# Performance work log

Measured on AMD Instinct MI355X. Metric: run time of the kernel, lower is better.

Reference implementation:

```python
import jax, jax.numpy as jnp
import numpy as np

B, S, J, D = 64, 2048, 25, 3
FEAT_DIM = 128
COMPUTED = 12  # pos(3) + vel(3) + acc(3) + angles(3)
IN_MLP = COMPUTED * J  # 300
HID = FEAT_DIM * 2     # 256
CONN = np.array([(0, 1), (1, 5), (1, 6), (5, 7), (7, 9), (6, 8), (8, 10),
                 (1, 11), (1, 12), (11, 13), (13, 15), (12, 14), (14, 16)], dtype=np.int32)


def setup_inputs() -> dict:
    key = jax.random.key(0)
    ks = jax.random.split(key, 8)
    return {
        "poses": jax.random.normal(ks[0], (B, S, J, D), dtype=jnp.float32),
        "W1": jax.random.normal(ks[1], (IN_MLP, HID), dtype=jnp.float32) * 0.05,
        "b1": jnp.zeros((HID,), jnp.float32),
        "gamma": jnp.ones((HID,), jnp.float32),
        "beta": jnp.zeros((HID,), jnp.float32),
        "running_mean": jnp.zeros((HID,), jnp.float32),
        "running_var": jnp.ones((HID,), jnp.float32),
        "W2": jax.random.normal(ks[2], (HID, FEAT_DIM), dtype=jnp.float32) * 0.05,
        "b2": jnp.zeros((FEAT_DIM,), jnp.float32),
        "joint_weights": jnp.ones((J,), jnp.float32),
    }


def reference(poses, W1, b1, gamma, beta, running_mean, running_var, W2, b2, joint_weights):
    b, s, j, d = poses.shape
    # --- root-centering + max-distance normalization ---
    p = poses - poses[:, :, 0:1, :]
    dist = jnp.linalg.norm(p, axis=-1, keepdims=True)           # [B,S,J,1]
    max_dist = jnp.max(dist, axis=2, keepdims=True)             # [B,S,1,1]
    p = p / (max_dist + 1e-8)
    # --- velocity / acceleration (zero-padded first frames) ---
    zpad = jnp.zeros_like(p[:, :1])
    vel = jnp.concatenate([zpad, p[:, 1:] - p[:, :-1]], axis=1)
    acc = jnp.concatenate([zpad, vel[:, 1:] - vel[:, :-1]], axis=1)
    # --- joint angles: vectorized gather + normalize + acos (replaces B*S*13 python loop) ---
    v1 = p[:, :, CONN[:, 1], :] - p[:, :, CONN[:, 0], :]        # [B,S,13,3]
    vnorm = jnp.maximum(jnp.linalg.norm(v1, axis=-1, keepdims=True), 1e-12)  # F.normalize eps
    ang = jnp.arccos(jnp.clip(v1 / vnorm, -1.0, 1.0))           # [B,S,13,3]
    ang = ang.reshape(b, s, -1)                                 # [B,S,39]
    pad = jnp.zeros((b, s, j * 3 - ang.shape[-1]), ang.dtype)   # pad to J*3=75
    angles = jnp.concatenate([ang, pad], axis=-1).reshape(b, s, j, 3)
    # --- combine, weight, project ---
    feat = jnp.concatenate([p, vel, acc, angles], axis=-1)      # [B,S,J,12]
    feat = feat * joint_weights.reshape(1, 1, j, 1)
    x = feat.reshape(b * s, -1)                                 # [B*S,300]
    x = x @ W1 + b1
    x = gamma * (x - running_mean) / jnp.sqrt(running_var + 1e-5) + beta  # BN eval mode
    x = jax.nn.relu(x)                                          # dropout = identity (eval)
    x = x @ W2 + b2
    return x.reshape(b, s, -1)                                  # [B,S,128]
```

## Files before the change

### kernel.cpp

```cpp
#include <hip/hip_runtime.h>
#include <hip/hip_bf16.h>
#include <stdint.h>


#define S_    2048
#define MT_   64
#define HID_  256
#define OUT_  128

typedef __attribute__((ext_vector_type(8))) short   short8;
typedef __attribute__((ext_vector_type(4))) float   floatx4;

#define C0M 0x0ECDB118675110ULL
#define C1M 0x0FDECBA9786540ULL

__device__ __forceinline__ unsigned short bf16_bits(float v) {
    union { float f; unsigned u; } x; x.f = v;
    unsigned r = x.u + 0x7fffu + ((x.u >> 16) & 1u);
    return (unsigned short)(r >> 16);
}

__device__ __forceinline__ unsigned pkbf16(float a, float b) {
#if __has_builtin(__builtin_amdgcn_cvt_pk_bf16_f32)
    auto v = __builtin_amdgcn_cvt_pk_bf16_f32(a, b);
    unsigned u; __builtin_memcpy(&u, &v, 4); return u;
#else
    return (unsigned)bf16_bits(a) | ((unsigned)bf16_bits(b) << 16);
#endif
}

__device__ __forceinline__ float facos(float x) {
    float ax = fabsf(x);
    float p = fmaf(ax, -0.0187293f, 0.0742610f);
    p = fmaf(ax, p, -0.2121144f);
    p = fmaf(ax, p, 1.5707288f);
    float r = __builtin_amdgcn_sqrtf(1.f - ax) * p;
    return x < 0.f ? 3.14159265358979f - r : r;
}

__global__ void prep_kernel(const float* __restrict__ W1, const float* __restrict__ b1,
                            const float* __restrict__ gamma, const float* __restrict__ beta,
                            const float* __restrict__ rmean, const float* __restrict__ rvar,
                            const float* __restrict__ W2,
                            unsigned short* __restrict__ w1p,
                            unsigned short* __restrict__ w2p,
                            float* __restrict__ b1p) {
    int idx = blockIdx.x * 256 + threadIdx.x;
    if (idx < 81920) {
        int k = idx >> 8, n = idx & 255;
        float a = gamma[n] * __builtin_amdgcn_rsqf(rvar[n] + 1e-5f);
        float v = (k < 300) ? W1[k * HID_ + n] * a : 0.f;
        int blk = (k >> 5) * 16 + (n >> 4);
        int off = blk * 512 + (((k >> 3) & 3) * 16 + (n & 15)) * 8 + (k & 7);
        w1p[off] = bf16_bits(v);
    } else if (idx < 114688) {
        int i2 = idx - 81920;
        int k = i2 >> 7, n = i2 & 127;
        int blk = (k >> 5) * 8 + (n >> 4);
        int off = blk * 512 + (((k >> 3) & 3) * 16 + (n & 15)) * 8 + (k & 7);
        w2p[off] = bf16_bits(W2[k * OUT_ + n]);
    } else if (idx < 114944) {
        int n = idx - 114688;
        float a = gamma[n] * __builtin_amdgcn_rsqf(rvar[n] + 1e-5f);
        b1p[n] = fmaf(a, b1[n] - rmean[n], beta[n]);
    }
}

#define LDS_FEAT 0
#define LDS_PB   41984
#define LDS_RSM  (LDS_PB + 34 * 76 * 4)
#define LDS_JW   (LDS_RSM + 34 * 4)
#define LDS_TOT  (LDS_JW + 25 * 4 + 4)

__global__ __launch_bounds__(256, 3) void pose_mlp(
    const float* __restrict__ poses,
    const unsigned short* __restrict__ w1p,
    const unsigned short* __restrict__ w2p,
    const float* __restrict__ b1p,
    const float* __restrict__ b2,
    const float* __restrict__ jw,
    float* __restrict__ out)
{
    __shared__ __align__(16) unsigned char smem[LDS_TOT];
    const int tid  = threadIdx.x;
    const int lane = tid & 63;
    const int wv   = tid >> 6;
    const int t0   = blockIdx.x * MT_;
    const int s0   = t0 & (S_ - 1);

    unsigned short* feat = (unsigned short*)(smem + LDS_FEAT);
    float*    pbuf = (float*)(smem + LDS_PB);
    unsigned* rsm  = (unsigned*)(smem + LDS_RSM);
    float*    scl  = (float*)rsm;
    float*    jwl  = (float*)(smem + LDS_JW);

    short8 bw[4];
    #pragma unroll
    for (int ni = 0; ni < 4; ni++)
        bw[ni] = *(const short8*)(w1p + (unsigned)(wv * 4 + ni) * 512 + lane * 8);

    if (tid < 25) jwl[tid] = jw[tid];
    for (int i = tid; i < MT_ * 64; i += 256) {
        int tt = i >> 6, z = i & 63;
        int k;
        if (z < 36) { int jj = z / 3; k = (13 + jj) * 12 + 9 + (z - jj * 3); }
        else        { k = 300 + z - 36; }
        feat[tt * 328 + k] = 0;
    }

    for (int h = 0; h < 2; h++) {
        int hb = t0 + 32 * h - 2;
        if (tid < 34) rsm[tid] = 0u;
        for (int i = tid; i < 34 * 75; i += 256) {
            int f = i / 75, r = i - f * 75;
            int g = hb + f; if (g < 0) g = 0;
            const float* P = poses + (size_t)g * 75;
            pbuf[f * 76 + r] = P[r] - P[r - (r / 3) * 3];
        }
        __syncthreads();
        for (int i = tid; i < 34 * 25; i += 256) {
            int f = i / 25, j = i - f * 25;
            const float* q = pbuf + f * 76 + j * 3;
            float d2 = fmaf(q[0], q[0], fmaf(q[1], q[1], q[2] * q[2]));
            atomicMax(&rsm[f], __float_as_uint(d2));
        }
        __syncthreads();
        if (tid < 34) {
            float m = __uint_as_float(rsm[tid]);
            scl[tid] = __builtin_amdgcn_rcpf(__builtin_amdgcn_sqrtf(m) + 1e-8f);
        }
        __syncthreads();
        for (int i = tid; i < 32 * 25; i += 256) {
            int tt = i / 25, j = i - tt * 25;
            int s  = s0 + 32 * h + tt;
            const float* pc = pbuf + (tt + 2) * 76 + j * 3;
            const float* pm = pc - 76;
            const float* pp = pc - 152;
            float sc = scl[tt + 2], sm = scl[tt + 1], sp = scl[tt];
            float cx = pc[0] * sc, cy = pc[1] * sc, cz = pc[2] * sc;
            float mx = pm[0] * sm, my = pm[1] * sm, mz = pm[2] * sm;
            float px = pp[0] * sp, py = pp[1] * sp, pz = pp[2] * sp;
            bool h1 = (s >= 1), h2 = (s >= 2);
            float vx = h1 ? cx - mx : 0.f, vy = h1 ? cy - my : 0.f, vz = h1 ? cz - mz : 0.f;
            float ux = h2 ? mx - px : 0.f, uy = h2 ? my - py : 0.f, uz = h2 ? mz - pz : 0.f;
            float qx = vx - ux, qy = vy - uy, qz = vz - uz;
            float w = jwl[j];
            unsigned base = (unsigned)(32 * h + tt) * 328 + j * 12;
            *(unsigned*)(feat + base)     = pkbf16(cx * w, cy * w);
            *(unsigned*)(feat + base + 2) = pkbf16(cz * w, vx * w);
            *(unsigned*)(feat + base + 4) = pkbf16(vy * w, vz * w);
            *(unsigned*)(feat + base + 6) = pkbf16(qx * w, qy * w);
            feat[base + 8] = bf16_bits(qz * w);
        }
        for (int i = tid; i < 32 * 13; i += 256) {
            int tt = i / 13, e = i - tt * 13;
            const float* pf = pbuf + (tt + 2) * 76;
            int a0 = (int)((C0M >> (4 * e)) & 15) * 3;
            int a1 = (((int)((C1M >> (4 * e)) & 15)) + 1) * 3;
            float vx = pf[a1] - pf[a0], vy = pf[a1+1] - pf[a0+1], vz = pf[a1+2] - pf[a0+2];
            float d  = fmaf(vx, vx, fmaf(vy, vy, vz * vz));
            float inv = __builtin_amdgcn_rcpf(fmaxf(__builtin_amdgcn_sqrtf(d), 1e-12f));
            float w = jwl[e];
            float A0 = facos(fminf(fmaxf(vx * inv, -1.f), 1.f)) * w;
            float A1 = facos(fminf(fmaxf(vy * inv, -1.f), 1.f)) * w;
            float A2 = facos(fminf(fmaxf(vz * inv, -1.f), 1.f)) * w;
            unsigned base = (unsigned)(32 * h + tt) * 328 + e * 12 + 9;
            feat[base] = bf16_bits(A0);
            *(unsigned*)(feat + base + 1) = pkbf16(A1, A2);
        }
        __syncthreads();
    }

    floatx4 acc[4][4];
    #pragma unroll
    for (int mi = 0; mi < 4; mi++)
        #pragma unroll
        for (int ni = 0; ni < 4; ni++) acc[mi][ni] = (floatx4){0.f, 0.f, 0.f, 0.f};

    #pragma unroll 1
    for (int kc = 0; kc < 10; kc++) {
        short8 bn[4];
        if (kc < 9) {
            #pragma unroll
            for (int ni = 0; ni < 4; ni++)
                bn[ni] = *(const short8*)(w1p + (unsigned)((kc + 1) * 16 + wv * 4 + ni) * 512 + lane * 8);
        }
        short8 af[4];
        #pragma unroll
        for (int mi = 0; mi < 4; mi++)
            af[mi] = *(const short8*)(feat + (mi * 16 + (lane & 15)) * 328 + kc * 32 + (lane >> 4) * 8);
        #pragma unroll
        for (int mi = 0; mi < 4; mi++)
            #pragma unroll
            for (int ni = 0; ni < 4; ni++)
                acc[mi][ni] = __builtin_amdgcn_mfma_f32_16x16x32_bf16(
                    af[mi], bw[ni], acc[mi][ni], 0, 0, 0);
        if (kc < 9) {
            #pragma unroll
            for (int ni = 0; ni < 4; ni++) bw[ni] = bn[ni];
        }
    }

    short8 bw2[2];
    #pragma unroll
    for (int ni = 0; ni < 2; ni++)
        bw2[ni] = *(const short8*)(w2p + (unsigned)(wv * 2 + ni) * 512 + lane * 8);

    __syncthreads();

    unsigned short* hid = feat;
    float bv[4];
    #pragma unroll
    for (int ni = 0; ni < 4; ni++) bv[ni] = b1p[wv * 64 + ni * 16 + (lane & 15)];
    #pragma unroll
    for (int mi = 0; mi < 4; mi++)
        #pragma unroll
        for (int ni = 0; ni < 4; ni++)
            #pragma unroll
            for (int r = 0; r < 4; r++) {
                float v = fmaxf(acc[mi][ni][r] + bv[ni], 0.f);
                int m   = mi * 16 + (lane >> 4) * 4 + r;
                int col = wv * 64 + ni * 16 + (lane & 15);
                hid[m * 264 + col] = bf16_bits(v);
            }
    __syncthreads();

    floatx4 acc2[4][2];
    #pragma unroll
    for (int mi = 0; mi < 4; mi++)
        #pragma unroll
        for (int ni = 0; ni < 2; ni++) acc2[mi][ni] = (floatx4){0.f, 0.f, 0.f, 0.f};

    #pragma unroll 1
    for (int kc = 0; kc < 8; kc++) {
        short8 bn2[2];
        if (kc < 7) {
            #pragma unroll
            for (int ni = 0; ni < 2; ni++)
                bn2[ni] = *(const short8*)(w2p + (unsigned)((kc + 1) * 8 + wv * 2 + ni) * 512 + lane * 8);
        }
        short8 af[4];
        #pragma unroll
        for (int mi = 0; mi < 4; mi++)
            af[mi] = *(const short8*)(hid + (mi * 16 + (lane & 15)) * 264 + kc * 32 + (lane >> 4) * 8);
        #pragma unroll
        for (int mi = 0; mi < 4; mi++)
            #pragma unroll
            for (int ni = 0; ni < 2; ni++)
                acc2[mi][ni] = __builtin_amdgcn_mfma_f32_16x16x32_bf16(
                    af[mi], bw2[ni], acc2[mi][ni], 0, 0, 0);
        if (kc < 7) {
            #pragma unroll
            for (int ni = 0; ni < 2; ni++) bw2[ni] = bn2[ni];
        }
    }

    float c2[2];
    #pragma unroll
    for (int ni = 0; ni < 2; ni++) c2[ni] = b2[wv * 32 + ni * 16 + (lane & 15)];
    #pragma unroll
    for (int mi = 0; mi < 4; mi++)
        #pragma unroll
        for (int ni = 0; ni < 2; ni++)
            #pragma unroll
            for (int r = 0; r < 4; r++) {
                int m   = mi * 16 + (lane >> 4) * 4 + r;
                int col = wv * 32 + ni * 16 + (lane & 15);
                out[(size_t)(t0 + m) * OUT_ + col] = acc2[mi][ni][r] + c2[ni];
            }
}

extern "C" void kernel_launch(void* const* d_in, const int* in_sizes, int n_in,
                              void* d_out, int out_size, void* d_ws, size_t ws_size,
                              hipStream_t stream) {
    (void)in_sizes; (void)n_in; (void)out_size; (void)ws_size;
    const float* poses = (const float*)d_in[0];
    const float* W1    = (const float*)d_in[1];
    const float* b1    = (const float*)d_in[2];
    const float* gamma = (const float*)d_in[3];
    const float* beta  = (const float*)d_in[4];
    const float* rmean = (const float*)d_in[5];
    const float* rvar  = (const float*)d_in[6];
    const float* W2    = (const float*)d_in[7];
    const float* b2    = (const float*)d_in[8];
    const float* jw    = (const float*)d_in[9];

    unsigned short* w1p = (unsigned short*)d_ws;
    unsigned short* w2p = w1p + 320 * HID_;
    float* b1p = (float*)((char*)d_ws + (320 * HID_ + HID_ * OUT_) * 2);

    prep_kernel<<<449, 256, 0, stream>>>(W1, b1, gamma, beta, rmean, rvar, W2,
                                         w1p, w2p, b1p);
    pose_mlp<<<2048, 256, 0, stream>>>(poses, w1p, w2p, b1p, b2, jw, (float*)d_out);
}
```

Measured before the change: 174.5 us.

## Use 512-thread blocks and compute pose features directly from global memory

Doubles the block to 8 waves, so each wave covers half as many output columns in both GEMMs (2 N-tiles instead of 4 for layer 1, 1 instead of 2 for layer 2). Feature construction moves from two staged 32-frame halves with an LDS pose buffer and atomicMax to one pass over all 66 frames. That pass computes a partial max per 5-joint group plus a per-frame root and scale record, then reads poses from global/L1 directly. The goal is fewer barriers and less LDS traffic, with more waves to hide latency. In exchange there are redundant global loads of poses, and each wave now re-reads the same A fragments for fewer MFMAs.

```diff
diff --git a/kernel.cpp b/kernel.cpp
--- a/kernel.cpp
+++ b/kernel.cpp
@@ -5,6 +5,7 @@
 
 #define S_    2048
 #define MT_   64
+#define TPB   512
 #define HID_  256
 #define OUT_  128
 
@@ -67,12 +68,12 @@
 }
 
 #define LDS_FEAT 0
-#define LDS_PB   41984
-#define LDS_RSM  (LDS_PB + 34 * 76 * 4)
-#define LDS_JW   (LDS_RSM + 34 * 4)
-#define LDS_TOT  (LDS_JW + 25 * 4 + 4)
-
-__global__ __launch_bounds__(256, 3) void pose_mlp(
+#define LDS_PM   41984
+#define LDS_RS   43312
+#define LDS_JW   (LDS_RS + 66 * 16)
+#define LDS_TOT  (LDS_JW + 25 * 4 + 12)
+
+__global__ __launch_bounds__(TPB, 6) void pose_mlp(
     const float* __restrict__ poses,
     const unsigned short* __restrict__ w1p,
     const unsigned short* __restrict__ w2p,
@@ -89,18 +90,17 @@
     const int s0   = t0 & (S_ - 1);
 
     unsigned short* feat = (unsigned short*)(smem + LDS_FEAT);
-    float*    pbuf = (float*)(smem + LDS_PB);
-    unsigned* rsm  = (unsigned*)(smem + LDS_RSM);
-    float*    scl  = (float*)rsm;
-    float*    jwl  = (float*)(smem + LDS_JW);
-
-    short8 bw[4];
-    #pragma unroll
-    for (int ni = 0; ni < 4; ni++)
-        bw[ni] = *(const short8*)(w1p + (unsigned)(wv * 4 + ni) * 512 + lane * 8);
+    float*  pm  = (float*)(smem + LDS_PM);
+    float4* rs  = (float4*)(smem + LDS_RS);
+    float*  jwl = (float*)(smem + LDS_JW);
+
+    short8 bw[2];
+    #pragma unroll
+    for (int ni = 0; ni < 2; ni++)
+        bw[ni] = *(const short8*)(w1p + (unsigned)(wv * 2 + ni) * 512 + lane * 8);
 
     if (tid < 25) jwl[tid] = jw[tid];
-    for (int i = tid; i < MT_ * 64; i += 256) {
+    for (int i = tid; i < MT_ * 64; i += TPB) {
         int tt = i >> 6, z = i & 63;
         int k;
         if (z < 36) { int jj = z / 3; k = (13 + jj) * 12 + 9 + (z - jj * 3); }
@@ -108,82 +108,91 @@
         feat[tt * 328 + k] = 0;
     }
 
-    for (int h = 0; h < 2; h++) {
-        int hb = t0 + 32 * h - 2;
-        if (tid < 34) rsm[tid] = 0u;
-        for (int i = tid; i < 34 * 75; i += 256) {
-            int f = i / 75, r = i - f * 75;
-            int g = hb + f; if (g < 0) g = 0;
-            const float* P = poses + (size_t)g * 75;
-            pbuf[f * 76 + r] = P[r] - P[r - (r / 3) * 3];
-        }
-        __syncthreads();
-        for (int i = tid; i < 34 * 25; i += 256) {
-            int f = i / 25, j = i - f * 25;
-            const float* q = pbuf + f * 76 + j * 3;
-            float d2 = fmaf(q[0], q[0], fmaf(q[1], q[1], q[2] * q[2]));
-            atomicMax(&rsm[f], __float_as_uint(d2));
-        }
-        __syncthreads();
-        if (tid < 34) {
-            float m = __uint_as_float(rsm[tid]);
-            scl[tid] = __builtin_amdgcn_rcpf(__builtin_amdgcn_sqrtf(m) + 1e-8f);
-        }
-        __syncthreads();
-        for (int i = tid; i < 32 * 25; i += 256) {
-            int tt = i / 25, j = i - tt * 25;
-            int s  = s0 + 32 * h + tt;
-            const float* pc = pbuf + (tt + 2) * 76 + j * 3;
-            const float* pm = pc - 76;
-            const float* pp = pc - 152;
-            float sc = scl[tt + 2], sm = scl[tt + 1], sp = scl[tt];
-            float cx = pc[0] * sc, cy = pc[1] * sc, cz = pc[2] * sc;
-            float mx = pm[0] * sm, my = pm[1] * sm, mz = pm[2] * sm;
-            float px = pp[0] * sp, py = pp[1] * sp, pz = pp[2] * sp;
-            bool h1 = (s >= 1), h2 = (s >= 2);
-            float vx = h1 ? cx - mx : 0.f, vy = h1 ? cy - my : 0.f, vz = h1 ? cz - mz : 0.f;
-            float ux = h2 ? mx - px : 0.f, uy = h2 ? my - py : 0.f, uz = h2 ? mz - pz : 0.f;
-            float qx = vx - ux, qy = vy - uy, qz = vz - uz;
-            float w = jwl[j];
-            unsigned base = (unsigned)(32 * h + tt) * 328 + j * 12;
-            *(unsigned*)(feat + base)     = pkbf16(cx * w, cy * w);
-            *(unsigned*)(feat + base + 2) = pkbf16(cz * w, vx * w);
-            *(unsigned*)(feat + base + 4) = pkbf16(vy * w, vz * w);
-            *(unsigned*)(feat + base + 6) = pkbf16(qx * w, qy * w);
-            feat[base + 8] = bf16_bits(qz * w);
-        }
-        for (int i = tid; i < 32 * 13; i += 256) {
-            int tt = i / 13, e = i - tt * 13;
-            const float* pf = pbuf + (tt + 2) * 76;
-            int a0 = (int)((C0M >> (4 * e)) & 15) * 3;
-            int a1 = (((int)((C1M >> (4 * e)) & 15)) + 1) * 3;
-            float vx = pf[a1] - pf[a0], vy = pf[a1+1] - pf[a0+1], vz = pf[a1+2] - pf[a0+2];
-            float d  = fmaf(vx, vx, fmaf(vy, vy, vz * vz));
-            float inv = __builtin_amdgcn_rcpf(fmaxf(__builtin_amdgcn_sqrtf(d), 1e-12f));
-            float w = jwl[e];
-            float A0 = facos(fminf(fmaxf(vx * inv, -1.f), 1.f)) * w;
-            float A1 = facos(fminf(fmaxf(vy * inv, -1.f), 1.f)) * w;
-            float A2 = facos(fminf(fmaxf(vz * inv, -1.f), 1.f)) * w;
-            unsigned base = (unsigned)(32 * h + tt) * 328 + e * 12 + 9;
-            feat[base] = bf16_bits(A0);
-            *(unsigned*)(feat + base + 1) = pkbf16(A1, A2);
-        }
-        __syncthreads();
-    }
-
-    floatx4 acc[4][4];
+    for (int i = tid; i < 66 * 5; i += TPB) {
+        int f = i / 5, grp = i - f * 5;
+        int g = t0 - 2 + f; if (g < 0) g = 0;
+        const float* P = poses + (size_t)g * 75;
+        float r0 = P[0], r1 = P[1], r2 = P[2];
+        float m2 = 0.f;
+        #pragma unroll
+        for (int jj = 0; jj < 5; jj++) {
+            int j = grp * 5 + jj;
+            float dx = P[j*3]   - r0;
+            float dy = P[j*3+1] - r1;
+            float dz = P[j*3+2] - r2;
+            m2 = fmaxf(m2, fmaf(dx, dx, fmaf(dy, dy, dz * dz)));
+        }
+        pm[i] = m2;
+    }
+    __syncthreads();
+    if (tid < 66) {
+        int g = t0 - 2 + tid; if (g < 0) g = 0;
+        const float* P = poses + (size_t)g * 75;
+        const float* q = pm + tid * 5;
+        float m2 = fmaxf(fmaxf(fmaxf(q[0], q[1]), fmaxf(q[2], q[3])), q[4]);
+        float sc = __builtin_amdgcn_rcpf(__builtin_amdgcn_sqrtf(m2) + 1e-8f);
+        rs[tid] = make_float4(P[0], P[1], P[2], sc);
+    }
+    __syncthreads();
+
+    for (int i = tid; i < MT_ * 25; i += TPB) {
+        int tt = i / 25, j = i - tt * 25;
+        int s  = s0 + tt;
+        int g  = t0 + tt;
+        int g1 = g - 1 < 0 ? 0 : g - 1;
+        int g2 = g - 2 < 0 ? 0 : g - 2;
+        const float* Pc = poses + (size_t)g  * 75 + j * 3;
+        const float* P1 = poses + (size_t)g1 * 75 + j * 3;
+        const float* P2 = poses + (size_t)g2 * 75 + j * 3;
+        float4 rc = rs[tt + 2], rm = rs[tt + 1], rp = rs[tt];
+        float cx = (Pc[0] - rc.x) * rc.w, cy = (Pc[1] - rc.y) * rc.w, cz = (Pc[2] - rc.z) * rc.w;
+        float mx = (P1[0] - rm.x) * rm.w, my = (P1[1] - rm.y) * rm.w, mz = (P1[2] - rm.z) * rm.w;
+        float px = (P2[0] - rp.x) * rp.w, py = (P2[1] - rp.y) * rp.w, pz = (P2[2] - rp.z) * rp.w;
+        bool h1 = (s >= 1), h2 = (s >= 2);
+        float vx = h1 ? cx - mx : 0.f, vy = h1 ? cy - my : 0.f, vz = h1 ? cz - mz : 0.f;
+        float ux = h2 ? mx - px : 0.f, uy = h2 ? my - py : 0.f, uz = h2 ? mz - pz : 0.f;
+        float qx = vx - ux, qy = vy - uy, qz = vz - uz;
+        float w = jwl[j];
+        unsigned base = (unsigned)tt * 328 + j * 12;
+        *(unsigned*)(feat + base)     = pkbf16(cx * w, cy * w);
+        *(unsigned*)(feat + base + 2) = pkbf16(cz * w, vx * w);
+        *(unsigned*)(feat + base + 4) = pkbf16(vy * w, vz * w);
+        *(unsigned*)(feat + base + 6) = pkbf16(qx * w, qy * w);
+        feat[base + 8] = bf16_bits(qz * w);
+    }
+
+    for (int i = tid; i < MT_ * 13; i += TPB) {
+        int tt = i / 13, e = i - tt * 13;
+        int g  = t0 + tt;
+        const float* P = poses + (size_t)g * 75;
+        int a0 = (int)((C0M >> (4 * e)) & 15) * 3;
+        int a1 = (((int)((C1M >> (4 * e)) & 15)) + 1) * 3;
+        float vx = P[a1] - P[a0], vy = P[a1+1] - P[a0+1], vz = P[a1+2] - P[a0+2];
+        float d  = fmaf(vx, vx, fmaf(vy, vy, vz * vz));
+        float inv = __builtin_amdgcn_rcpf(fmaxf(__builtin_amdgcn_sqrtf(d), 1e-12f));
+        float w = jwl[e];
+        float A0 = facos(fminf(fmaxf(vx * inv, -1.f), 1.f)) * w;
+        float A1 = facos(fminf(fmaxf(vy * inv, -1.f), 1.f)) * w;
+        float A2 = facos(fminf(fmaxf(vz * inv, -1.f), 1.f)) * w;
+        unsigned base = (unsigned)tt * 328 + e * 12 + 9;
+        feat[base] = bf16_bits(A0);
+        *(unsigned*)(feat + base + 1) = pkbf16(A1, A2);
+    }
+    __syncthreads();
+
+    floatx4 acc[4][2];
     #pragma unroll
     for (int mi = 0; mi < 4; mi++)
         #pragma unroll
-        for (int ni = 0; ni < 4; ni++) acc[mi][ni] = (floatx4){0.f, 0.f, 0.f, 0.f};
+        for (int ni = 0; ni < 2; ni++) acc[mi][ni] = (floatx4){0.f, 0.f, 0.f, 0.f};
 
     #pragma unroll 1
     for (int kc = 0; kc < 10; kc++) {
-        short8 bn[4];
+        short8 bn[2];
         if (kc < 9) {
             #pragma unroll
-            for (int ni = 0; ni < 4; ni++)
-                bn[ni] = *(const short8*)(w1p + (unsigned)((kc + 1) * 16 + wv * 4 + ni) * 512 + lane * 8);
+            for (int ni = 0; ni < 2; ni++)
+                bn[ni] = *(const short8*)(w1p + (unsigned)((kc + 1) * 16 + wv * 2 + ni) * 512 + lane * 8);
         }
         short8 af[4];
         #pragma unroll
@@ -192,82 +201,65 @@
         #pragma unroll
         for (int mi = 0; mi < 4; mi++)
             #pragma unroll
-            for (int ni = 0; ni < 4; ni++)
+            for (int ni = 0; ni < 2; ni++)
                 acc[mi][ni] = __builtin_amdgcn_mfma_f32_16x16x32_bf16(
                     af[mi], bw[ni], acc[mi][ni], 0, 0, 0);
         if (kc < 9) {
             #pragma unroll
-            for (int ni = 0; ni < 4; ni++) bw[ni] = bn[ni];
-        }
-    }
-
-    short8 bw2[2];
-    #pragma unroll
-    for (int ni = 0; ni < 2; ni++)
-        bw2[ni] = *(const short8*)(w2p + (unsigned)(wv * 2 + ni) * 512 + lane * 8);
+            for (int ni = 0; ni < 2; ni++) bw[ni] = bn[ni];
+        }
+    }
+
+    short8 bw2 = *(const short8*)(w2p + (unsigned)wv * 512 + lane * 8);
 
     __syncthreads();
 
     unsigned short* hid = feat;
-    float bv[4];
-    #pragma unroll
-    for (int ni = 0; ni < 4; ni++) bv[ni] = b1p[wv * 64 + ni * 16 + (lane & 15)];
+    float bv[2];
+    #pragma unroll
+    for (int ni = 0; ni < 2; ni++) bv[ni] = b1p[wv * 32 + ni * 16 + (lane & 15)];
     #pragma unroll
     for (int mi = 0; mi < 4; mi++)
         #pragma unroll
-        for (int ni = 0; ni < 4; ni++)
+        for (int ni = 0; ni < 2; ni++)
             #pragma unroll
             for (int r = 0; r < 4; r++) {
                 float v = fmaxf(acc[mi][ni][r] + bv[ni], 0.f);
                 int m   = mi * 16 + (lane >> 4) * 4 + r;
-                int col = wv * 64 + ni * 16 + (lane & 15);
+                int col = wv * 32 + ni * 16 + (lane & 15);
                 hid[m * 264 + col] = bf16_bits(v);
             }
     __syncthreads();
 
-    floatx4 acc2[4][2];
-    #pragma unroll
-    for (int mi = 0; mi < 4; mi++)
-        #pragma unroll
-        for (int ni = 0; ni < 2; ni++) acc2[mi][ni] = (floatx4){0.f, 0.f, 0.f, 0.f};
+    floatx4 acc2[4];
+    #pragma unroll
+    for (int mi = 0; mi < 4; mi++) acc2[mi] = (floatx4){0.f, 0.f, 0.f, 0.f};
 
     #pragma unroll 1
     for (int kc = 0; kc < 8; kc++) {
-        short8 bn2[2];
-        if (kc < 7) {
-            #pragma unroll
-            for (int ni = 0; ni < 2; ni++)
-                bn2[ni] = *(const short8*)(w2p + (unsigned)((kc + 1) * 8 + wv * 2 + ni) * 512 + lane * 8);
-        }
+        short8 bn2;
+        if (kc < 7)
+            bn2 = *(const short8*)(w2p + (unsigned)((kc + 1) * 8 + wv) * 512 + lane * 8);
         short8 af[4];
         #pragma unroll
         for (int mi = 0; mi < 4; mi++)
             af[mi] = *(const short8*)(hid + (mi * 16 + (lane & 15)) * 264 + kc * 32 + (lane >> 4) * 8);
         #pragma unroll
         for (int mi = 0; mi < 4; mi++)
-            #pragma unroll
-            for (int ni = 0; ni < 2; ni++)
-                acc2[mi][ni] = __builtin_amdgcn_mfma_f32_16x16x32_bf16(
-                    af[mi], bw2[ni], acc2[mi][ni], 0, 0, 0);
-        if (kc < 7) {
-            #pragma unroll
-            for (int ni = 0; ni < 2; ni++) bw2[ni] = bn2[ni];
-        }
-    }
-
-    float c2[2];
-    #pragma unroll
-    for (int ni = 0; ni < 2; ni++) c2[ni] = b2[wv * 32 + ni * 16 + (lane & 15)];
+            acc2[mi] = __builtin_amdgcn_mfma_f32_16x16x32_bf16(
+                af[mi], bw2, acc2[mi], 0, 0, 0);
+        if (kc < 7) bw2 = bn2;
+    }
+
+    float c2 = b2[wv * 16 + (lane & 15)];
     #pragma unroll
     for (int mi = 0; mi < 4; mi++)
         #pragma unroll
-        for (int ni = 0; ni < 2; ni++)
-            #pragma unroll
-            for (int r = 0; r < 4; r++) {
-                int m   = mi * 16 + (lane >> 4) * 4 + r;
-                int col = wv * 32 + ni * 16 + (lane & 15);
-                out[(size_t)(t0 + m) * OUT_ + col] = acc2[mi][ni][r] + c2[ni];
-            }
+        for (int r = 0; r < 4; r++) {
+            int m   = mi * 16 + (lane >> 4) * 4 + r;
+            int col = wv * 16 + (lane & 15);
+            out[(size_t)(t0 + m) * OUT_ + col] = acc2[mi][r] + c2;
+        }
 }
 
 extern "C" void kernel_launch(void* const* d_in, const int* in_sizes, int n_in,
@@ -291,5 +283,5 @@
 
     prep_kernel<<<449, 256, 0, stream>>>(W1, b1, gamma, beta, rmean, rvar, W2,
                                          w1p, w2p, b1p);
-    pose_mlp<<<2048, 256, 0, stream>>>(poses, w1p, w2p, b1p, b2, jw, (float*)d_out);
-}
+    pose_mlp<<<2048, TPB, 0, stream>>>(poses, w1p, w2p, b1p, b2, jw, (float*)d_out);
+}
```

Result: faster. 144.4 us (-17.3%).
